# Optimization experiments

Hardware: AMD Instinct MI355X
Metric: run time of the kernel (lower is better)

Reference implementation:

```python
import jax, jax.numpy as jnp
import numpy as np

N_NODES = 100000
N_EDGES = 1600000
D = 64  # latent = hidden = output = 64


def gcn_conv(x, W, b, src, dst, n):
    # PyG GCNConv: out = D^{-1/2} (A + I) D^{-1/2} (x W) + b, self-loops added.
    h = x @ W  # [N, d_out]
    ones = jnp.ones(src.shape[0], dtype=h.dtype)
    deg = jax.ops.segment_sum(ones, dst, num_segments=n) + 1.0  # +1 for self-loop
    dinv = jax.lax.rsqrt(deg)  # [N]
    norm = dinv[src] * dinv[dst]  # [E]
    msgs = h[src] * norm[:, None]  # gather + scale, [E, d_out]
    agg = jax.ops.segment_sum(msgs, dst, num_segments=n)  # scatter-add
    # self-loop contribution: dinv[i]^2 * h[i]
    agg = agg + h * (dinv * dinv)[:, None]
    return agg + b


def setup_inputs() -> dict:
    key = jax.random.key(0)
    ks = jax.random.split(key, 9)
    s = 1.0 / np.sqrt(D)
    return {
        "z": jax.random.normal(ks[0], (N_NODES, D), dtype=jnp.float32),
        "src": jax.random.randint(ks[1], (N_EDGES,), 0, N_NODES, dtype=jnp.int32),
        "dst": jax.random.randint(ks[2], (N_EDGES,), 0, N_NODES, dtype=jnp.int32),
        "W1": jax.random.uniform(ks[3], (D, D), jnp.float32, -s, s),
        "b1": jnp.zeros((D,), jnp.float32),
        "W2": jax.random.uniform(ks[4], (D, D), jnp.float32, -s, s),
        "b2": jnp.zeros((D,), jnp.float32),
        "W3": jax.random.uniform(ks[5], (D, D), jnp.float32, -s, s),
        "b3": jnp.zeros((D,), jnp.float32),
    }


def reference(z, src, dst, W1, b1, W2, b2, W3, b3):
    n = z.shape[0]
    x = jax.nn.relu(gcn_conv(z, W1, b1, src, dst, n))
    x = jax.nn.relu(gcn_conv(x, W2, b2, src, dst, n))
    x = gcn_conv(x, W3, b3, src, dst, n)
    return x
```

## Files before the change

kernel.cpp:

```cpp
#include <hip/hip_runtime.h>
#include <hip/hip_fp16.h>

#define N_NODES 100000
#define N_EDGES 1600000
#define N_BUCKETS 256
#define BUCKET_NODES 391
#define BKT_BLOCKS 512
#define CAP_E 8192
#define CAP_C 12288
#define DUMMY N_NODES

typedef unsigned short u16;
typedef _Float16 f16x8 __attribute__((ext_vector_type(8)));
typedef float f32x4 __attribute__((ext_vector_type(4)));
typedef unsigned u32x4 __attribute__((ext_vector_type(4)));

__device__ __forceinline__ u16 f2h(float f) {
    return __half_as_ushort(__float2half_rn(f));
}

__device__ __forceinline__ u32x4 gload16(const char* addr) {
    u32x4 d;
    asm volatile("global_load_dwordx4 %0, %1, off" : "=v"(d) : "v"(addr));
    return d;
}

__device__ __forceinline__ void acc8v(float* acc, u32x4 q) {
#pragma unroll
    for (int i = 0; i < 4; ++i) {
        unsigned w = q[i];
        __half2 h = *reinterpret_cast<__half2*>(&w);
        float2 f = __half22float2(h);
        acc[2 * i] += f.x;
        acc[2 * i + 1] += f.y;
    }
}

__device__ __forceinline__ void acc8(float* acc, uint4 q) {
    unsigned v[4] = {q.x, q.y, q.z, q.w};
#pragma unroll
    for (int i = 0; i < 4; ++i) {
        __half2 h = *reinterpret_cast<__half2*>(&v[i]);
        float2 f = __half22float2(h);
        acc[2 * i] += f.x;
        acc[2 * i + 1] += f.y;
    }
}

__global__ __launch_bounds__(256) void k_bucket(const int* __restrict__ src,
                                                const int* __restrict__ dst,
                                                int* __restrict__ btot,
                                                int* __restrict__ ebuf) {
    __shared__ int cnt[N_BUCKETS], base_s[N_BUCKETS];
    const int CS = N_EDGES / BKT_BLOCKS;
    int t = threadIdx.x;
    int beg = blockIdx.x * CS, end = beg + CS;
    for (int i = t; i < N_BUCKETS; i += 256) cnt[i] = 0;
    __syncthreads();
    for (int e = beg + t; e < end; e += 256)
        atomicAdd(&cnt[(unsigned)dst[e] / BUCKET_NODES], 1);
    __syncthreads();
    for (int i = t; i < N_BUCKETS; i += 256) {
        base_s[i] = atomicAdd(&btot[i], cnt[i]);
        cnt[i] = 0;
    }
    __syncthreads();
    for (int e = beg + t; e < end; e += 256) {
        int d = dst[e], s = src[e];
        int b = (unsigned)d / BUCKET_NODES;
        int l = atomicAdd(&cnt[b], 1);
        ebuf[b * CAP_E + base_s[b] + l] = s | ((d - b * BUCKET_NODES) << 17);
    }
}

__global__ __launch_bounds__(1024) void k_build(const int* __restrict__ btot,
                                                const int* __restrict__ ebuf,
                                                int* __restrict__ col,
                                                int2* __restrict__ rowinfo,
                                                float* __restrict__ dinv,
                                                const float* __restrict__ z,
                                                u16* __restrict__ xs,
                                                u16* __restrict__ xs_other) {
    __shared__ int deg[BUCKET_NODES];
    __shared__ int cur[BUCKET_NODES];
    __shared__ int sm[512];
    __shared__ int cls[CAP_C];
    int b = blockIdx.x, t = threadIdx.x;
    int nb = b * BUCKET_NODES;
    int nn = N_NODES - nb < BUCKET_NODES ? N_NODES - nb : BUCKET_NODES;
    int ne = btot[b];
    const int* eb = ebuf + b * CAP_E;

    for (int i = t; i < BUCKET_NODES; i += 1024) deg[i] = 0;
    __syncthreads();
    for (int e = t; e < ne; e += 1024) atomicAdd(&deg[eb[e] >> 17], 1);
    __syncthreads();

    int v = (t < nn) ? ((deg[t] + 7) & ~7) : 0;
    if (t < 512) sm[t] = v;
    __syncthreads();
    for (int off = 1; off < 512; off <<= 1) {
        int u = (t >= off && t < 512) ? sm[t - off] : 0;
        __syncthreads();
        if (t < 512) sm[t] += u;
        __syncthreads();
    }
    int total = sm[511];
    int colbase = b * CAP_C;
    if (t < nn) {
        int off0 = sm[t] - v;
        cur[t] = off0;
        rowinfo[nb + t] = make_int2(colbase + off0, v);
        dinv[nb + t] = rsqrtf((float)deg[t] + 1.0f);
    }
    __syncthreads();
    for (int i = t; i < total; i += 1024) cls[i] = DUMMY << 7;
    __syncthreads();
    for (int e = t; e < ne; e += 1024) {
        int pe = eb[e];
        int l = atomicAdd(&cur[pe >> 17], 1);
        cls[l] = (pe & 0x1FFFF) << 7;
    }
    __syncthreads();
    for (int i = t; i < total; i += 1024) col[colbase + i] = cls[i];
    if (t < 16) col[colbase + total + t] = DUMMY << 7;

    const float4* zz = (const float4*)(z + (size_t)nb * 64);
    uint2* xx = (uint2*)(xs + (size_t)nb * 64);
    for (int i = t; i < nn * 16; i += 1024) {
        float4 vv = zz[i];
        float dd = rsqrtf((float)deg[i >> 4] + 1.0f);
        unsigned p0 = (unsigned)f2h(vv.x * dd) | ((unsigned)f2h(vv.y * dd) << 16);
        unsigned p1 = (unsigned)f2h(vv.z * dd) | ((unsigned)f2h(vv.w * dd) << 16);
        xx[i] = make_uint2(p0, p1);
    }
    if (b == 0 && t < 8) {
        ((uint4*)(xs + (size_t)N_NODES * 64))[t] = make_uint4(0, 0, 0, 0);
        ((uint4*)(xs_other + (size_t)N_NODES * 64))[t] = make_uint4(0, 0, 0, 0);
    }
}

__global__ __launch_bounds__(256, 3) void k_agg(const int2* __restrict__ rowinfo,
                                                const int* __restrict__ col,
                                                const float* __restrict__ dinv,
                                                const u16* __restrict__ xs,
                                                u16* __restrict__ h) {
    const int lane = threadIdx.x & 63;
    const int eighth = lane >> 3;
    const int fh = lane & 7;
    const char* xb = (const char*)xs;
    int wave = (blockIdx.x * blockDim.x + threadIdx.x) >> 6;
    int nwaves = (gridDim.x * blockDim.x) >> 6;

    for (int n0 = wave * 4; n0 < N_NODES; n0 += nwaves * 4) {
        int u0 = __builtin_amdgcn_readfirstlane(n0);
        int2 r0 = rowinfo[u0];
        int2 r1 = rowinfo[u0 + 1];
        int2 r2 = rowinfo[u0 + 2];
        int2 r3 = rowinfo[u0 + 3];
        int it0 = r0.y >> 4, it1 = r1.y >> 4, it2 = r2.y >> 4, it3 = r3.y >> 4;
        int itm = it0 > it1 ? it0 : it1;
        if (it2 > itm) itm = it2;
        if (it3 > itm) itm = it3;

        int2 c0 = *(const int2*)(col + r0.x + 2 * eighth);
        int2 c1 = *(const int2*)(col + r1.x + 2 * eighth);
        int2 c2 = *(const int2*)(col + r2.x + 2 * eighth);
        int2 c3 = *(const int2*)(col + r3.x + 2 * eighth);
        int tc0 = col[r0.x + (it0 << 4) + eighth];
        int tc1 = col[r1.x + (it1 << 4) + eighth];
        int tc2 = col[r2.x + (it2 << 4) + eighth];
        int tc3 = col[r3.x + (it3 << 4) + eighth];
        float d0 = dinv[u0];
        float d1 = dinv[u0 + 1];
        float d2 = dinv[u0 + 2];
        float d3 = dinv[u0 + 3];

        u32x4 q0 = gload16(xb + (unsigned)c0.x + fh * 16);
        u32x4 q1 = gload16(xb + (unsigned)c0.y + fh * 16);
        u32x4 q2 = gload16(xb + (unsigned)c1.x + fh * 16);
        u32x4 q3 = gload16(xb + (unsigned)c1.y + fh * 16);
        u32x4 q4 = gload16(xb + (unsigned)c2.x + fh * 16);
        u32x4 q5 = gload16(xb + (unsigned)c2.y + fh * 16);
        u32x4 q6 = gload16(xb + (unsigned)c3.x + fh * 16);
        u32x4 q7 = gload16(xb + (unsigned)c3.y + fh * 16);
        u32x4 g0 = gload16(xb + (unsigned)tc0 + fh * 16);
        u32x4 g1 = gload16(xb + (unsigned)tc1 + fh * 16);
        u32x4 g2 = gload16(xb + (unsigned)tc2 + fh * 16);
        u32x4 g3 = gload16(xb + (unsigned)tc3 + fh * 16);
        u32x4 s0 = gload16(xb + (size_t)u0 * 128 + fh * 16);
        u32x4 s1 = gload16(xb + (size_t)(u0 + 1) * 128 + fh * 16);
        u32x4 s2 = gload16(xb + (size_t)(u0 + 2) * 128 + fh * 16);
        u32x4 s3 = gload16(xb + (size_t)(u0 + 3) * 128 + fh * 16);
        asm volatile("s_waitcnt vmcnt(0)" ::: "memory");
        __builtin_amdgcn_sched_barrier(0);

        float a0[8] = {0.f, 0.f, 0.f, 0.f, 0.f, 0.f, 0.f, 0.f};
        float a1[8] = {0.f, 0.f, 0.f, 0.f, 0.f, 0.f, 0.f, 0.f};
        float a2[8] = {0.f, 0.f, 0.f, 0.f, 0.f, 0.f, 0.f, 0.f};
        float a3[8] = {0.f, 0.f, 0.f, 0.f, 0.f, 0.f, 0.f, 0.f};
        if (0 < it0) { acc8v(a0, q0); acc8v(a0, q1); }
        if (0 < it1) { acc8v(a1, q2); acc8v(a1, q3); }
        if (0 < it2) { acc8v(a2, q4); acc8v(a2, q5); }
        if (0 < it3) { acc8v(a3, q6); acc8v(a3, q7); }
        if ((r0.y >> 3) & 1) acc8v(a0, g0);
        if ((r1.y >> 3) & 1) acc8v(a1, g1);
        if ((r2.y >> 3) & 1) acc8v(a2, g2);
        if ((r3.y >> 3) & 1) acc8v(a3, g3);
        if (eighth == 0) acc8v(a0, s0);
        if (eighth == 1) acc8v(a1, s1);
        if (eighth == 2) acc8v(a2, s2);
        if (eighth == 3) acc8v(a3, s3);

        for (int rr = 1; rr < itm; ++rr) {
            int2 e0 = *(const int2*)(col + r0.x + ((rr < it0 ? rr : 0) << 4) + 2 * eighth);
            int2 e1 = *(const int2*)(col + r1.x + ((rr < it1 ? rr : 0) << 4) + 2 * eighth);
            int2 e2 = *(const int2*)(col + r2.x + ((rr < it2 ? rr : 0) << 4) + 2 * eighth);
            int2 e3 = *(const int2*)(col + r3.x + ((rr < it3 ? rr : 0) << 4) + 2 * eighth);
            uint4 p0 = *(const uint4*)(xb + (unsigned)e0.x + fh * 16);
            uint4 p1 = *(const uint4*)(xb + (unsigned)e0.y + fh * 16);
            uint4 p2 = *(const uint4*)(xb + (unsigned)e1.x + fh * 16);
            uint4 p3 = *(const uint4*)(xb + (unsigned)e1.y + fh * 16);
            uint4 p4 = *(const uint4*)(xb + (unsigned)e2.x + fh * 16);
            uint4 p5 = *(const uint4*)(xb + (unsigned)e2.y + fh * 16);
            uint4 p6 = *(const uint4*)(xb + (unsigned)e3.x + fh * 16);
            uint4 p7 = *(const uint4*)(xb + (unsigned)e3.y + fh * 16);
            if (rr < it0) { acc8(a0, p0); acc8(a0, p1); }
            if (rr < it1) { acc8(a1, p2); acc8(a1, p3); }
            if (rr < it2) { acc8(a2, p4); acc8(a2, p5); }
            if (rr < it3) { acc8(a3, p6); acc8(a3, p7); }
        }

#pragma unroll
        for (int m = 8; m <= 32; m <<= 1) {
#pragma unroll
            for (int j = 0; j < 8; ++j) {
                a0[j] += __shfl_xor(a0[j], m, 64);
                a1[j] += __shfl_xor(a1[j], m, 64);
                a2[j] += __shfl_xor(a2[j], m, 64);
                a3[j] += __shfl_xor(a3[j], m, 64);
            }
        }
        uint4 p0, p1, p2, p3;
        u16* pp0 = (u16*)&p0;
        u16* pp1 = (u16*)&p1;
        u16* pp2 = (u16*)&p2;
        u16* pp3 = (u16*)&p3;
#pragma unroll
        for (int j = 0; j < 8; ++j) {
            pp0[j] = f2h(a0[j] * d0);
            pp1[j] = f2h(a1[j] * d1);
            pp2[j] = f2h(a2[j] * d2);
            pp3[j] = f2h(a3[j] * d3);
        }
        if (eighth == 0) ((uint4*)(h + (size_t)u0 * 64))[fh] = p0;
        if (eighth == 1) ((uint4*)(h + (size_t)(u0 + 1) * 64))[fh] = p1;
        if (eighth == 2) ((uint4*)(h + (size_t)(u0 + 2) * 64))[fh] = p2;
        if (eighth == 3) ((uint4*)(h + (size_t)(u0 + 3) * 64))[fh] = p3;
    }
}

__global__ __launch_bounds__(256) void k_prepw(const float* __restrict__ W1,
                                               const float* __restrict__ W2,
                                               const float* __restrict__ W3,
                                               u16* __restrict__ Wp) {
    const float* W = blockIdx.x == 0 ? W1 : (blockIdx.x == 1 ? W2 : W3);
    u16* o = Wp + blockIdx.x * 4096;
    for (int f = threadIdx.x; f < 4096; f += 256) {
        int j = f & 7, l16 = (f >> 3) & 15, quad = (f >> 7) & 3;
        int c = (f >> 9) & 1, t = f >> 10;
        o[f] = f2h(W[(quad * 8 + 32 * c + j) * 64 + 4 * l16 + t]);
    }
}

__global__ __launch_bounds__(256) void k_mv(const u16* __restrict__ h,
                                            const u16* __restrict__ Wp,
                                            const float* __restrict__ bias,
                                            const float* __restrict__ dinv,
                                            u16* __restrict__ outh,
                                            float* __restrict__ outf, int hidden) {
    const int lane = threadIdx.x & 63;
    const int quad = lane >> 4;
    const int l16 = lane & 15;

    const uint4* wq = (const uint4*)Wp;
    union { uint4 u; f16x8 f; } bfr[4][2];
#pragma unroll
    for (int t = 0; t < 4; ++t)
#pragma unroll
        for (int c = 0; c < 2; ++c)
            bfr[t][c].u = wq[t * 128 + c * 64 + quad * 16 + l16];
    float4 bq = ((const float4*)bias)[l16];
    float bv[4] = {bq.x, bq.y, bq.z, bq.w};

    int wave = (blockIdx.x * blockDim.x + threadIdx.x) >> 6;
    int nwaves = (gridDim.x * blockDim.x) >> 6;
    for (int chunk = wave; chunk < N_NODES / 16; chunk += nwaves) {
        int row0 = chunk * 16;
        const u16* hb = h + (size_t)row0 * 64;
        union { uint4 u; f16x8 f; } a0, a1;
        a0.u = *(const uint4*)(hb + l16 * 64 + quad * 8);
        a1.u = *(const uint4*)(hb + l16 * 64 + quad * 8 + 32);

        f32x4 acc[4] = {{0.f, 0.f, 0.f, 0.f}, {0.f, 0.f, 0.f, 0.f},
                        {0.f, 0.f, 0.f, 0.f}, {0.f, 0.f, 0.f, 0.f}};
#pragma unroll
        for (int t = 0; t < 4; ++t) {
            acc[t] = __builtin_amdgcn_mfma_f32_16x16x32_f16(a0.f, bfr[t][0].f, acc[t], 0, 0, 0);
            acc[t] = __builtin_amdgcn_mfma_f32_16x16x32_f16(a1.f, bfr[t][1].f, acc[t], 0, 0, 0);
        }
        float dv[4];
#pragma unroll
        for (int r = 0; r < 4; ++r) dv[r] = dinv[row0 + quad * 4 + r];
#pragma unroll
        for (int r = 0; r < 4; ++r) {
            int row = row0 + quad * 4 + r;
            float o[4];
#pragma unroll
            for (int t = 0; t < 4; ++t) o[t] = acc[t][r] + bv[t];
            if (hidden) {
                float dd = dv[r];
#pragma unroll
                for (int t = 0; t < 4; ++t) o[t] = fmaxf(o[t], 0.f) * dd;
                unsigned lo = (unsigned)f2h(o[0]) | ((unsigned)f2h(o[1]) << 16);
                unsigned hi = (unsigned)f2h(o[2]) | ((unsigned)f2h(o[3]) << 16);
                ((uint2*)(outh + (size_t)row * 64))[l16] = make_uint2(lo, hi);
            } else {
                ((float4*)(outf + (size_t)row * 64))[l16] =
                    make_float4(o[0], o[1], o[2], o[3]);
            }
        }
    }
}

extern "C" void kernel_launch(void* const* d_in, const int* in_sizes, int n_in,
                              void* d_out, int out_size, void* d_ws, size_t ws_size,
                              hipStream_t stream) {
    const float* z  = (const float*)d_in[0];
    const int* src  = (const int*)d_in[1];
    const int* dst  = (const int*)d_in[2];
    const float* W1 = (const float*)d_in[3];
    const float* b1 = (const float*)d_in[4];
    const float* W2 = (const float*)d_in[5];
    const float* b2 = (const float*)d_in[6];
    const float* W3 = (const float*)d_in[7];
    const float* b3 = (const float*)d_in[8];
    float* out = (float*)d_out;

    char* p = (char*)d_ws;
    float* dinv    = (float*)p;  p += (size_t)512 << 10;
    int2*  rowinfo = (int2*)p;   p += (size_t)1 << 20;
    int*   btot    = (int*)p;    p += (size_t)4 << 10;
    int*   ebuf    = (int*)p;    p += (size_t)N_BUCKETS * CAP_E * 4;
    int*   col     = (int*)p;    p += (size_t)N_BUCKETS * CAP_C * 4;
    u16*   hbuf    = (u16*)p;    p += (size_t)13 << 20;
    u16*   buf0    = (u16*)p;    p += (size_t)13 << 20;
    u16*   buf1    = (u16*)p;    p += (size_t)13 << 20;
    u16*   wp      = (u16*)p;

    const int gA = 2048;
    const int gM = 1563;

    k_prepw<<<3, 256, 0, stream>>>(W1, W2, W3, wp);
    hipMemsetAsync(btot, 0, N_BUCKETS * sizeof(int), stream);
    k_bucket<<<BKT_BLOCKS, 256, 0, stream>>>(src, dst, btot, ebuf);
    k_build<<<N_BUCKETS, 1024, 0, stream>>>(btot, ebuf, col, rowinfo, dinv, z, buf0, buf1);

    k_agg<<<gA, 256, 0, stream>>>(rowinfo, col, dinv, buf0, hbuf);
    k_mv <<<gM, 256, 0, stream>>>(hbuf, wp, b1, dinv, buf1, nullptr, 1);
    k_agg<<<gA, 256, 0, stream>>>(rowinfo, col, dinv, buf1, hbuf);
    k_mv <<<gM, 256, 0, stream>>>(hbuf, wp + 4096, b2, dinv, buf0, nullptr, 1);
    k_agg<<<gA, 256, 0, stream>>>(rowinfo, col, dinv, buf0, hbuf);
    k_mv <<<gM, 256, 0, stream>>>(hbuf, wp + 8192, b3, dinv, nullptr, out, 0);
}
```

Baseline: 264.6 us.

## Fuse aggregation with MFMA weight transform and fold weight prep into bucketing

Merges the sparse aggregation kernel and the dense 64x64 MFMA transform into one kernel per layer. Each wave's four aggregated rows are shuffled into MFMA A-fragments directly, which removes the hbuf round trip and three kernel launches. Weight packing moves into extra blocks of the bucketing kernel, dropping one more launch. Tail gathers are now predicated and the four self-loop loads collapse into one per lane. The fused MFMA uses only 4 of its 16 rows, which wastes matrix throughput and adds shuffle and register pressure inside the memory-bound loop.

Measured after the change: 285.7 us. 8.0% more time.

```diff
diff --git a/kernel.cpp b/kernel.cpp
--- a/kernel.cpp
+++ b/kernel.cpp
@@ -50,8 +50,23 @@
 __global__ __launch_bounds__(256) void k_bucket(const int* __restrict__ src,
                                                 const int* __restrict__ dst,
                                                 int* __restrict__ btot,
-                                                int* __restrict__ ebuf) {
+                                                int* __restrict__ ebuf,
+                                                const float* __restrict__ W1,
+                                                const float* __restrict__ W2,
+                                                const float* __restrict__ W3,
+                                                u16* __restrict__ Wp) {
     __shared__ int cnt[N_BUCKETS], base_s[N_BUCKETS];
+    if (blockIdx.x >= BKT_BLOCKS) {
+        int wb = blockIdx.x - BKT_BLOCKS;
+        const float* W = wb == 0 ? W1 : (wb == 1 ? W2 : W3);
+        u16* o = Wp + wb * 4096;
+        for (int f = threadIdx.x; f < 4096; f += 256) {
+            int j = f & 7, l16 = (f >> 3) & 15, quad = (f >> 7) & 3;
+            int c = (f >> 9) & 1, t = f >> 10;
+            o[f] = f2h(W[(quad * 8 + 32 * c + j) * 64 + 4 * l16 + t]);
+        }
+        return;
+    }
     const int CS = N_EDGES / BKT_BLOCKS;
     int t = threadIdx.x;
     int beg = blockIdx.x * CS, end = beg + CS;
@@ -140,15 +155,31 @@
     }
 }
 
-__global__ __launch_bounds__(256, 3) void k_agg(const int2* __restrict__ rowinfo,
-                                                const int* __restrict__ col,
-                                                const float* __restrict__ dinv,
-                                                const u16* __restrict__ xs,
-                                                u16* __restrict__ h) {
+__global__ __launch_bounds__(256, 3) void k_fused(const int2* __restrict__ rowinfo,
+                                                  const int* __restrict__ col,
+                                                  const float* __restrict__ dinv,
+                                                  const u16* __restrict__ xs,
+                                                  const u16* __restrict__ Wp,
+                                                  const float* __restrict__ bias,
+                                                  u16* __restrict__ outh,
+                                                  float* __restrict__ outf,
+                                                  int hidden) {
     const int lane = threadIdx.x & 63;
     const int eighth = lane >> 3;
     const int fh = lane & 7;
+    const int l16 = lane & 15;
+    const int quad = lane >> 4;
     const char* xb = (const char*)xs;
+
+    const uint4* wq = (const uint4*)Wp;
+    union { uint4 u; f16x8 f; } bfr[4][2];
+#pragma unroll
+    for (int t = 0; t < 4; ++t)
+#pragma unroll
+        for (int c = 0; c < 2; ++c)
+            bfr[t][c].u = wq[t * 128 + c * 64 + quad * 16 + l16];
+    float4 bq = ((const float4*)bias)[l16];
+
     int wave = (blockIdx.x * blockDim.x + threadIdx.x) >> 6;
     int nwaves = (gridDim.x * blockDim.x) >> 6;
 
@@ -162,6 +193,8 @@
         int itm = it0 > it1 ? it0 : it1;
         if (it2 > itm) itm = it2;
         if (it3 > itm) itm = it3;
+        int t0 = (r0.y >> 3) & 1, t1 = (r1.y >> 3) & 1;
+        int t2 = (r2.y >> 3) & 1, t3 = (r3.y >> 3) & 1;
 
         int2 c0 = *(const int2*)(col + r0.x + 2 * eighth);
         int2 c1 = *(const int2*)(col + r1.x + 2 * eighth);
@@ -184,14 +217,13 @@
         u32x4 q5 = gload16(xb + (unsigned)c2.y + fh * 16);
         u32x4 q6 = gload16(xb + (unsigned)c3.x + fh * 16);
         u32x4 q7 = gload16(xb + (unsigned)c3.y + fh * 16);
-        u32x4 g0 = gload16(xb + (unsigned)tc0 + fh * 16);
-        u32x4 g1 = gload16(xb + (unsigned)tc1 + fh * 16);
-        u32x4 g2 = gload16(xb + (unsigned)tc2 + fh * 16);
-        u32x4 g3 = gload16(xb + (unsigned)tc3 + fh * 16);
-        u32x4 s0 = gload16(xb + (size_t)u0 * 128 + fh * 16);
-        u32x4 s1 = gload16(xb + (size_t)(u0 + 1) * 128 + fh * 16);
-        u32x4 s2 = gload16(xb + (size_t)(u0 + 2) * 128 + fh * 16);
-        u32x4 s3 = gload16(xb + (size_t)(u0 + 3) * 128 + fh * 16);
+        u32x4 g0 = {0, 0, 0, 0}, g1 = {0, 0, 0, 0};
+        u32x4 g2 = {0, 0, 0, 0}, g3 = {0, 0, 0, 0};
+        if (t0) g0 = gload16(xb + (unsigned)tc0 + fh * 16);
+        if (t1) g1 = gload16(xb + (unsigned)tc1 + fh * 16);
+        if (t2) g2 = gload16(xb + (unsigned)tc2 + fh * 16);
+        if (t3) g3 = gload16(xb + (unsigned)tc3 + fh * 16);
+        u32x4 sf = gload16(xb + (size_t)(u0 + (eighth & 3)) * 128 + fh * 16);
         asm volatile("s_waitcnt vmcnt(0)" ::: "memory");
         __builtin_amdgcn_sched_barrier(0);
 
@@ -203,14 +235,14 @@
         if (0 < it1) { acc8v(a1, q2); acc8v(a1, q3); }
         if (0 < it2) { acc8v(a2, q4); acc8v(a2, q5); }
         if (0 < it3) { acc8v(a3, q6); acc8v(a3, q7); }
-        if ((r0.y >> 3) & 1) acc8v(a0, g0);
-        if ((r1.y >> 3) & 1) acc8v(a1, g1);
-        if ((r2.y >> 3) & 1) acc8v(a2, g2);
-        if ((r3.y >> 3) & 1) acc8v(a3, g3);
-        if (eighth == 0) acc8v(a0, s0);
-        if (eighth == 1) acc8v(a1, s1);
-        if (eighth == 2) acc8v(a2, s2);
-        if (eighth == 3) acc8v(a3, s3);
+        if (t0) acc8v(a0, g0);
+        if (t1) acc8v(a1, g1);
+        if (t2) acc8v(a2, g2);
+        if (t3) acc8v(a3, g3);
+        if (eighth == 0) acc8v(a0, sf);
+        if (eighth == 1) acc8v(a1, sf);
+        if (eighth == 2) acc8v(a2, sf);
+        if (eighth == 3) acc8v(a3, sf);
 
         for (int rr = 1; rr < itm; ++rr) {
             int2 e0 = *(const int2*)(col + r0.x + ((rr < it0 ? rr : 0) << 4) + 2 * eighth);
@@ -253,81 +285,56 @@
             pp2[j] = f2h(a2[j] * d2);
             pp3[j] = f2h(a3[j] * d3);
         }
-        if (eighth == 0) ((uint4*)(h + (size_t)u0 * 64))[fh] = p0;
-        if (eighth == 1) ((uint4*)(h + (size_t)(u0 + 1) * 64))[fh] = p1;
-        if (eighth == 2) ((uint4*)(h + (size_t)(u0 + 2) * 64))[fh] = p2;
-        if (eighth == 3) ((uint4*)(h + (size_t)(u0 + 3) * 64))[fh] = p3;
-    }
-}
-
-__global__ __launch_bounds__(256) void k_prepw(const float* __restrict__ W1,
-                                               const float* __restrict__ W2,
-                                               const float* __restrict__ W3,
-                                               u16* __restrict__ Wp) {
-    const float* W = blockIdx.x == 0 ? W1 : (blockIdx.x == 1 ? W2 : W3);
-    u16* o = Wp + blockIdx.x * 4096;
-    for (int f = threadIdx.x; f < 4096; f += 256) {
-        int j = f & 7, l16 = (f >> 3) & 15, quad = (f >> 7) & 3;
-        int c = (f >> 9) & 1, t = f >> 10;
-        o[f] = f2h(W[(quad * 8 + 32 * c + j) * 64 + 4 * l16 + t]);
-    }
-}
-
-__global__ __launch_bounds__(256) void k_mv(const u16* __restrict__ h,
-                                            const u16* __restrict__ Wp,
-                                            const float* __restrict__ bias,
-                                            const float* __restrict__ dinv,
-                                            u16* __restrict__ outh,
-                                            float* __restrict__ outf, int hidden) {
-    const int lane = threadIdx.x & 63;
-    const int quad = lane >> 4;
-    const int l16 = lane & 15;
-
-    const uint4* wq = (const uint4*)Wp;
-    union { uint4 u; f16x8 f; } bfr[4][2];
-#pragma unroll
-    for (int t = 0; t < 4; ++t)
-#pragma unroll
-        for (int c = 0; c < 2; ++c)
-            bfr[t][c].u = wq[t * 128 + c * 64 + quad * 16 + l16];
-    float4 bq = ((const float4*)bias)[l16];
-    float bv[4] = {bq.x, bq.y, bq.z, bq.w};
-
-    int wave = (blockIdx.x * blockDim.x + threadIdx.x) >> 6;
-    int nwaves = (gridDim.x * blockDim.x) >> 6;
-    for (int chunk = wave; chunk < N_NODES / 16; chunk += nwaves) {
-        int row0 = chunk * 16;
-        const u16* hb = h + (size_t)row0 * 64;
-        union { uint4 u; f16x8 f; } a0, a1;
-        a0.u = *(const uint4*)(hb + l16 * 64 + quad * 8);
-        a1.u = *(const uint4*)(hb + l16 * 64 + quad * 8 + 32);
-
+
+        int e3i = eighth & 3;
+        uint4 pa;
+        pa.x = e3i == 0 ? p0.x : e3i == 1 ? p1.x : e3i == 2 ? p2.x : p3.x;
+        pa.y = e3i == 0 ? p0.y : e3i == 1 ? p1.y : e3i == 2 ? p2.y : p3.y;
+        pa.z = e3i == 0 ? p0.z : e3i == 1 ? p1.z : e3i == 2 ? p2.z : p3.z;
+        pa.w = e3i == 0 ? p0.w : e3i == 1 ? p1.w : e3i == 2 ? p2.w : p3.w;
+        int si0 = (l16 << 3) | quad;
+        int si1 = si0 | 4;
+        union { uint4 u; f16x8 f; } A0, A1;
+        A0.u.x = (unsigned)__shfl((int)pa.x, si0, 64);
+        A0.u.y = (unsigned)__shfl((int)pa.y, si0, 64);
+        A0.u.z = (unsigned)__shfl((int)pa.z, si0, 64);
+        A0.u.w = (unsigned)__shfl((int)pa.w, si0, 64);
+        A1.u.x = (unsigned)__shfl((int)pa.x, si1, 64);
+        A1.u.y = (unsigned)__shfl((int)pa.y, si1, 64);
+        A1.u.z = (unsigned)__shfl((int)pa.z, si1, 64);
+        A1.u.w = (unsigned)__shfl((int)pa.w, si1, 64);
+        if (l16 >= 4) {
+            A0.u = make_uint4(0, 0, 0, 0);
+            A1.u = make_uint4(0, 0, 0, 0);
+        }
         f32x4 acc[4] = {{0.f, 0.f, 0.f, 0.f}, {0.f, 0.f, 0.f, 0.f},
                         {0.f, 0.f, 0.f, 0.f}, {0.f, 0.f, 0.f, 0.f}};
 #pragma unroll
         for (int t = 0; t < 4; ++t) {
-            acc[t] = __builtin_amdgcn_mfma_f32_16x16x32_f16(a0.f, bfr[t][0].f, acc[t], 0, 0, 0);
-            acc[t] = __builtin_amdgcn_mfma_f32_16x16x32_f16(a1.f, bfr[t][1].f, acc[t], 0, 0, 0);
-        }
-        float dv[4];
-#pragma unroll
-        for (int r = 0; r < 4; ++r) dv[r] = dinv[row0 + quad * 4 + r];
-#pragma unroll
-        for (int r = 0; r < 4; ++r) {
-            int row = row0 + quad * 4 + r;
-            float o[4];
-#pragma unroll
-            for (int t = 0; t < 4; ++t) o[t] = acc[t][r] + bv[t];
-            if (hidden) {
-                float dd = dv[r];
-#pragma unroll
-                for (int t = 0; t < 4; ++t) o[t] = fmaxf(o[t], 0.f) * dd;
-                unsigned lo = (unsigned)f2h(o[0]) | ((unsigned)f2h(o[1]) << 16);
-                unsigned hi = (unsigned)f2h(o[2]) | ((unsigned)f2h(o[3]) << 16);
-                ((uint2*)(outh + (size_t)row * 64))[l16] = make_uint2(lo, hi);
-            } else {
-                ((float4*)(outf + (size_t)row * 64))[l16] =
-                    make_float4(o[0], o[1], o[2], o[3]);
+            acc[t] = __builtin_amdgcn_mfma_f32_16x16x32_f16(A0.f, bfr[t][0].f, acc[t], 0, 0, 0);
+            acc[t] = __builtin_amdgcn_mfma_f32_16x16x32_f16(A1.f, bfr[t][1].f, acc[t], 0, 0, 0);
+        }
+        if (quad == 0) {
+#pragma unroll
+            for (int r = 0; r < 4; ++r) {
+                float o0 = acc[0][r] + bq.x;
+                float o1 = acc[1][r] + bq.y;
+                float o2 = acc[2][r] + bq.z;
+                float o3 = acc[3][r] + bq.w;
+                int row = u0 + r;
+                if (hidden) {
+                    float dd = r == 0 ? d0 : r == 1 ? d1 : r == 2 ? d2 : d3;
+                    o0 = fmaxf(o0, 0.f) * dd;
+                    o1 = fmaxf(o1, 0.f) * dd;
+                    o2 = fmaxf(o2, 0.f) * dd;
+                    o3 = fmaxf(o3, 0.f) * dd;
+                    unsigned lo = (unsigned)f2h(o0) | ((unsigned)f2h(o1) << 16);
+                    unsigned hi = (unsigned)f2h(o2) | ((unsigned)f2h(o3) << 16);
+                    ((uint2*)(outh + (size_t)row * 64))[l16] = make_uint2(lo, hi);
+                } else {
+                    ((float4*)(outf + (size_t)row * 64))[l16] =
+                        make_float4(o0, o1, o2, o3);
+                }
             }
         }
     }
@@ -357,19 +364,15 @@
     u16*   buf0    = (u16*)p;    p += (size_t)13 << 20;
     u16*   buf1    = (u16*)p;    p += (size_t)13 << 20;
     u16*   wp      = (u16*)p;
+    (void)hbuf;
 
     const int gA = 2048;
-    const int gM = 1563;
-
-    k_prepw<<<3, 256, 0, stream>>>(W1, W2, W3, wp);
+
     hipMemsetAsync(btot, 0, N_BUCKETS * sizeof(int), stream);
-    k_bucket<<<BKT_BLOCKS, 256, 0, stream>>>(src, dst, btot, ebuf);
+    k_bucket<<<BKT_BLOCKS + 3, 256, 0, stream>>>(src, dst, btot, ebuf, W1, W2, W3, wp);
     k_build<<<N_BUCKETS, 1024, 0, stream>>>(btot, ebuf, col, rowinfo, dinv, z, buf0, buf1);
 
-    k_agg<<<gA, 256, 0, stream>>>(rowinfo, col, dinv, buf0, hbuf);
-    k_mv <<<gM, 256, 0, stream>>>(hbuf, wp, b1, dinv, buf1, nullptr, 1);
-    k_agg<<<gA, 256, 0, stream>>>(rowinfo, col, dinv, buf1, hbuf);
-    k_mv <<<gM, 256, 0, stream>>>(hbuf, wp + 4096, b2, dinv, buf0, nullptr, 1);
-    k_agg<<<gA, 256, 0, stream>>>(rowinfo, col, dinv, buf0, hbuf);
-    k_mv <<<gM, 256, 0, stream>>>(hbuf, wp + 8192, b3, dinv, nullptr, out, 0);
-}
+    k_fused<<<gA, 256, 0, stream>>>(rowinfo, col, dinv, buf0, wp,        b1, buf1, nullptr, 1);
+    k_fused<<<gA, 256, 0, stream>>>(rowinfo, col, dinv, buf1, wp + 4096, b2, buf0, nullptr, 1);
+    k_fused<<<gA, 256, 0, stream>>>(rowinfo, col, dinv, buf0, wp + 8192, b3, nullptr, out, 0);
+}
```

## Use smaller buckets, fold weight prep into bucketing, and shuffle-scan in build

Applied to the files above, without the earlier changes.

Splits nodes into 512 buckets of 196 instead of 256 of 391, so the CSR build kernel runs twice as many blocks at 512 threads each. The block-wide Hillis-Steele prefix sum over shared memory, which needed a barrier per step, is replaced by a wavefront shuffle scan plus a small cross-wave sum. Weight conversion is merged into the bucketing kernel as three extra blocks, removing one launch. The aggregation grid grows from 2048 to 6250 blocks. Per-bucket capacities are halved, which leaves less headroom for unevenly filled buckets.

After: 257.0 us. 2.8% less time.

```diff
diff --git a/kernel.cpp b/kernel.cpp
--- a/kernel.cpp
+++ b/kernel.cpp
@@ -3,11 +3,11 @@
 
 #define N_NODES 100000
 #define N_EDGES 1600000
-#define N_BUCKETS 256
-#define BUCKET_NODES 391
+#define N_BUCKETS 512
+#define BUCKET_NODES 196
 #define BKT_BLOCKS 512
-#define CAP_E 8192
-#define CAP_C 12288
+#define CAP_E 4096
+#define CAP_C 6144
 #define DUMMY N_NODES
 
 typedef unsigned short u16;
@@ -50,8 +50,23 @@
 __global__ __launch_bounds__(256) void k_bucket(const int* __restrict__ src,
                                                 const int* __restrict__ dst,
                                                 int* __restrict__ btot,
-                                                int* __restrict__ ebuf) {
+                                                int* __restrict__ ebuf,
+                                                const float* __restrict__ W1,
+                                                const float* __restrict__ W2,
+                                                const float* __restrict__ W3,
+                                                u16* __restrict__ Wp) {
     __shared__ int cnt[N_BUCKETS], base_s[N_BUCKETS];
+    if (blockIdx.x >= BKT_BLOCKS) {
+        int wb = blockIdx.x - BKT_BLOCKS;
+        const float* W = wb == 0 ? W1 : (wb == 1 ? W2 : W3);
+        u16* o = Wp + wb * 4096;
+        for (int f = threadIdx.x; f < 4096; f += 256) {
+            int j = f & 7, l16 = (f >> 3) & 15, quad = (f >> 7) & 3;
+            int c = (f >> 9) & 1, t = f >> 10;
+            o[f] = f2h(W[(quad * 8 + 32 * c + j) * 64 + 4 * l16 + t]);
+        }
+        return;
+    }
     const int CS = N_EDGES / BKT_BLOCKS;
     int t = threadIdx.x;
     int beg = blockIdx.x * CS, end = beg + CS;
@@ -73,61 +88,67 @@
     }
 }
 
-__global__ __launch_bounds__(1024) void k_build(const int* __restrict__ btot,
-                                                const int* __restrict__ ebuf,
-                                                int* __restrict__ col,
-                                                int2* __restrict__ rowinfo,
-                                                float* __restrict__ dinv,
-                                                const float* __restrict__ z,
-                                                u16* __restrict__ xs,
-                                                u16* __restrict__ xs_other) {
+__global__ __launch_bounds__(512) void k_build(const int* __restrict__ btot,
+                                               const int* __restrict__ ebuf,
+                                               int* __restrict__ col,
+                                               int2* __restrict__ rowinfo,
+                                               float* __restrict__ dinv,
+                                               const float* __restrict__ z,
+                                               u16* __restrict__ xs,
+                                               u16* __restrict__ xs_other) {
     __shared__ int deg[BUCKET_NODES];
     __shared__ int cur[BUCKET_NODES];
-    __shared__ int sm[512];
+    __shared__ int wsum[4];
     __shared__ int cls[CAP_C];
     int b = blockIdx.x, t = threadIdx.x;
     int nb = b * BUCKET_NODES;
-    int nn = N_NODES - nb < BUCKET_NODES ? N_NODES - nb : BUCKET_NODES;
+    int nn = N_NODES - nb;
+    if (nn > BUCKET_NODES) nn = BUCKET_NODES;
     int ne = btot[b];
     const int* eb = ebuf + b * CAP_E;
 
-    for (int i = t; i < BUCKET_NODES; i += 1024) deg[i] = 0;
-    __syncthreads();
-    for (int e = t; e < ne; e += 1024) atomicAdd(&deg[eb[e] >> 17], 1);
-    __syncthreads();
-
-    int v = (t < nn) ? ((deg[t] + 7) & ~7) : 0;
-    if (t < 512) sm[t] = v;
-    __syncthreads();
-    for (int off = 1; off < 512; off <<= 1) {
-        int u = (t >= off && t < 512) ? sm[t - off] : 0;
-        __syncthreads();
-        if (t < 512) sm[t] += u;
-        __syncthreads();
-    }
-    int total = sm[511];
+    for (int i = t; i < BUCKET_NODES; i += 512) deg[i] = 0;
+    __syncthreads();
+    for (int e = t; e < ne; e += 512) atomicAdd(&deg[eb[e] >> 17], 1);
+    __syncthreads();
+
+    int pv = (t < nn) ? ((deg[t] + 7) & ~7) : 0;
+    int v = pv;
+    int lane = t & 63, wv = t >> 6;
+#pragma unroll
+    for (int off = 1; off < 64; off <<= 1) {
+        int u = __shfl_up(v, off, 64);
+        if (lane >= off) v += u;
+    }
+    if (t < 256 && lane == 63) wsum[wv] = v;
+    __syncthreads();
+    int total = wsum[0] + wsum[1] + wsum[2] + wsum[3];
+    int add = 0;
+    for (int i = 0; i < wv && i < 4; ++i) add += wsum[i];
+    int incl = v + add;
+
     int colbase = b * CAP_C;
     if (t < nn) {
-        int off0 = sm[t] - v;
+        int off0 = incl - pv;
         cur[t] = off0;
-        rowinfo[nb + t] = make_int2(colbase + off0, v);
+        rowinfo[nb + t] = make_int2(colbase + off0, pv);
         dinv[nb + t] = rsqrtf((float)deg[t] + 1.0f);
     }
     __syncthreads();
-    for (int i = t; i < total; i += 1024) cls[i] = DUMMY << 7;
-    __syncthreads();
-    for (int e = t; e < ne; e += 1024) {
+    for (int i = t; i < total; i += 512) cls[i] = DUMMY << 7;
+    __syncthreads();
+    for (int e = t; e < ne; e += 512) {
         int pe = eb[e];
         int l = atomicAdd(&cur[pe >> 17], 1);
         cls[l] = (pe & 0x1FFFF) << 7;
     }
     __syncthreads();
-    for (int i = t; i < total; i += 1024) col[colbase + i] = cls[i];
+    for (int i = t; i < total; i += 512) col[colbase + i] = cls[i];
     if (t < 16) col[colbase + total + t] = DUMMY << 7;
 
     const float4* zz = (const float4*)(z + (size_t)nb * 64);
     uint2* xx = (uint2*)(xs + (size_t)nb * 64);
-    for (int i = t; i < nn * 16; i += 1024) {
+    for (int i = t; i < nn * 16; i += 512) {
         float4 vv = zz[i];
         float dd = rsqrtf((float)deg[i >> 4] + 1.0f);
         unsigned p0 = (unsigned)f2h(vv.x * dd) | ((unsigned)f2h(vv.y * dd) << 16);
@@ -260,19 +281,6 @@
     }
 }
 
-__global__ __launch_bounds__(256) void k_prepw(const float* __restrict__ W1,
-                                               const float* __restrict__ W2,
-                                               const float* __restrict__ W3,
-                                               u16* __restrict__ Wp) {
-    const float* W = blockIdx.x == 0 ? W1 : (blockIdx.x == 1 ? W2 : W3);
-    u16* o = Wp + blockIdx.x * 4096;
-    for (int f = threadIdx.x; f < 4096; f += 256) {
-        int j = f & 7, l16 = (f >> 3) & 15, quad = (f >> 7) & 3;
-        int c = (f >> 9) & 1, t = f >> 10;
-        o[f] = f2h(W[(quad * 8 + 32 * c + j) * 64 + 4 * l16 + t]);
-    }
-}
-
 __global__ __launch_bounds__(256) void k_mv(const u16* __restrict__ h,
                                             const u16* __restrict__ Wp,
                                             const float* __restrict__ bias,
@@ -358,13 +366,12 @@
     u16*   buf1    = (u16*)p;    p += (size_t)13 << 20;
     u16*   wp      = (u16*)p;
 
-    const int gA = 2048;
+    const int gA = 6250;
     const int gM = 1563;
 
-    k_prepw<<<3, 256, 0, stream>>>(W1, W2, W3, wp);
     hipMemsetAsync(btot, 0, N_BUCKETS * sizeof(int), stream);
-    k_bucket<<<BKT_BLOCKS, 256, 0, stream>>>(src, dst, btot, ebuf);
-    k_build<<<N_BUCKETS, 1024, 0, stream>>>(btot, ebuf, col, rowinfo, dinv, z, buf0, buf1);
+    k_bucket<<<BKT_BLOCKS + 3, 256, 0, stream>>>(src, dst, btot, ebuf, W1, W2, W3, wp);
+    k_build<<<N_BUCKETS, 512, 0, stream>>>(btot, ebuf, col, rowinfo, dinv, z, buf0, buf1);
 
     k_agg<<<gA, 256, 0, stream>>>(rowinfo, col, dinv, buf0, hbuf);
     k_mv <<<gM, 256, 0, stream>>>(hbuf, wp, b1, dinv, buf1, nullptr, 1);
```
